# Optimization experiments

Hardware: AMD Instinct MI355X
Metric: run time of the kernel (lower is better)

The kernel has to match this reference:

```python
import jax, jax.numpy as jnp
import numpy as np

NUM_HEADS = 20
MAX_SEQLEN = 1500  # max per-segment length (Whisper 30s -> 1500 frames); static for jit
NEG = -1e30


def setup_inputs() -> dict:
    key = jax.random.key(0)
    ks = jax.random.split(key, 6)
    B, S, D = 4, MAX_SEQLEN, 1280
    T = B * S
    hidden_states = jax.random.normal(ks[0], (T, D), dtype=jnp.float32)
    # packed varlen layout: 4 equal-length audio segments
    cu_seqlens = (jnp.arange(B + 1, dtype=jnp.int32) * S)
    w = 0.02
    Wq = jax.random.normal(ks[1], (D, D), dtype=jnp.float32) * w
    Wk = jax.random.normal(ks[2], (D, D), dtype=jnp.float32) * w
    Wv = jax.random.normal(ks[3], (D, D), dtype=jnp.float32) * w
    Wo = jax.random.normal(ks[4], (D, D), dtype=jnp.float32) * w
    bq = jnp.zeros((D,), jnp.float32)
    bv = jnp.zeros((D,), jnp.float32)
    bo = jnp.zeros((D,), jnp.float32)
    return {"hidden_states": hidden_states, "cu_seqlens": cu_seqlens,
            "Wq": Wq, "bq": bq, "Wk": Wk, "Wv": Wv, "bv": bv, "Wo": Wo, "bo": bo}


def _varlen_attention(hidden_states, cu_seqlens, Wq, bq, Wk, Wv, bv, Wo, bo):
    T, D = hidden_states.shape
    H = NUM_HEADS
    d = D // H
    scale = d ** -0.5
    S = MAX_SEQLEN
    B = cu_seqlens.shape[0] - 1

    # projections (torch nn.Linear convention: y = x @ W.T + b; k_proj has no bias)
    q = hidden_states @ Wq.T + bq   # [T, D]
    k = hidden_states @ Wk.T        # [T, D]
    v = hidden_states @ Wv.T + bv   # [T, D]

    lens = cu_seqlens[1:] - cu_seqlens[:-1]                 # [B]
    pos = jnp.arange(S, dtype=jnp.int32)                    # [S]
    valid = pos[None, :] < lens[:, None]                    # [B, S]
    idx = cu_seqlens[:-1, None] + pos[None, :]              # [B, S]
    idx_g = jnp.where(valid, idx, 0)

    # unpack to padded [B, S, H, d]
    qb = q[idx_g].reshape(B, S, H, d)
    kb = k[idx_g].reshape(B, S, H, d)
    vb = v[idx_g].reshape(B, S, H, d)

    scores = jnp.einsum('bqhd,bkhd->bhqk', qb, kb) * scale  # [B, H, S, S]
    scores = jnp.where(valid[:, None, None, :], scores, NEG)
    attn = jax.nn.softmax(scores, axis=-1)
    out = jnp.einsum('bhqk,bkhd->bqhd', attn, vb).reshape(B, S, D)

    # repack to [T, D]; invalid slots scatter out-of-bounds and are dropped
    idx_s = jnp.where(valid, idx, T).reshape(-1)
    packed = jnp.zeros((T, D), out.dtype).at[idx_s].set(out.reshape(-1, D), mode='drop')
    return packed @ Wo.T + bo


def reference(hidden_states, cu_seqlens, Wq, bq, Wk, Wv, bv, Wo, bo):
    return _varlen_attention(hidden_states, cu_seqlens, Wq, bq, Wk, Wv, bv, Wo, bo)
```

## Files before the change

### kernel.cpp

```cpp
#include <hip/hip_runtime.h>
#include <stdint.h>
#include <math.h>

#define DMODEL 1280
#define NHEAD  20
#define DHEAD  64
#define NSEG   4
#define MAXS   1500
#define SPAD   1536
#define TPAD   (NSEG*SPAD)
#define QT128  ((MAXS + 127) / 128)
#define BM 128
#define BN 128
#define BK 32
#define QSCALE 0.18033688011112042f
#define NEGV  -1e30f

typedef float  f32x4  __attribute__((ext_vector_type(4)));
typedef __bf16 bf16x8 __attribute__((ext_vector_type(8)));

#if __has_builtin(__builtin_amdgcn_exp2f)
#define EXP2F(x) __builtin_amdgcn_exp2f(x)
#else
#define EXP2F(x) exp2f(x)
#endif

__device__ __forceinline__ ushort f2bf(float f) {
  union { float f; uint32_t u; } a; a.f = f;
  uint32_t u = a.u;
  u += 0x7FFFu + ((u >> 16) & 1u);
  return (ushort)(u >> 16);
}

__device__ __forceinline__ uint32_t pk2(float a, float b) {
  union { float f; uint32_t u; } ua, ub; ua.f = a; ub.f = b;
  uint32_t x = ua.u + 0x8000u, y = ub.u + 0x8000u;
  return (x >> 16) | (y & 0xFFFF0000u);
}

__device__ __forceinline__ void async16(const void* g, void* lds) {
  __builtin_amdgcn_global_load_lds((const __attribute__((address_space(1))) void*)g,
                                   (__attribute__((address_space(3))) void*)lds,
                                   16, 0, 0);
}

__device__ __forceinline__ int perm32(int a) {
  return ((a >> 2) & 3) * 8 + ((a >> 4) & 1) * 4 + (a & 3);
}

__global__ void __launch_bounds__(256)
cvt_all(const float* __restrict__ hs, const float* __restrict__ Wq,
        const float* __restrict__ Wk, const float* __restrict__ Wv,
        const float* __restrict__ Wo, ushort* __restrict__ dst, int nX, int DD) {
  const int i = (blockIdx.x * 256 + threadIdx.x) * 4;
  const float* src;
  if (i < nX) {
    src = hs + i;
  } else {
    int j = i - nX;
    const int z = (j >= DD) + (j >= 2 * DD) + (j >= 3 * DD);
    const float* w = (z == 0) ? Wq : (z == 1) ? Wk : (z == 2) ? Wv : Wo;
    src = w + (j - z * DD);
  }
  float4 v = *(const float4*)src;
  ushort4 o;
  o.x = f2bf(v.x); o.y = f2bf(v.y); o.z = f2bf(v.z); o.w = f2bf(v.w);
  *(ushort4*)(dst + i) = o;
}

__device__ __forceinline__ void gemm_tile_mainloop(
    const ushort* __restrict__ A, const ushort* __restrict__ W,
    int M, int m0, int n0, ushort* As, ushort* Bs, f32x4 (&acc)[4][4])
{
  const int tid  = threadIdx.x;
  const int wave = tid >> 6, lane = tid & 63;
  const int quad = lane >> 4, c16 = lane & 15;
  const int wr = (wave >> 1) * 64, wc = (wave & 1) * 64;

  const int M0 = wave * 128 + lane, M1 = M0 + 64;
  const int sr0 = M0 >> 3, pp0 = M0 & 7, p0 = pp0 ^ (sr0 & 7);
  const int sr1 = M1 >> 3, pp1 = M1 & 7, p1 = pp1 ^ (sr1 & 7);
  const int row0 = sr0 * 2 + (p0 >> 2), kc0 = (p0 & 3) << 3;
  const int row1 = sr1 * 2 + (p1 >> 2), kc1 = (p1 & 3) << 3;
  const ushort* Ap0 = A + (size_t)(m0 + row0) * DMODEL + kc0;
  const ushort* Ap1 = A + (size_t)(m0 + row1) * DMODEL + kc1;
  const ushort* Bp0 = W + (size_t)(n0 + row0) * DMODEL + kc0;
  const ushort* Bp1 = W + (size_t)(n0 + row1) * DMODEL + kc1;
  const int o0 = wave * 1024;
  const int o1 = wave * 1024 + 512;
  const int BUF = BM * BK;

  async16(Ap0, As + o0); async16(Ap1, As + o1);
  async16(Bp0, Bs + o0); async16(Bp1, Bs + o1);

  int c = 0;
  for (int k0 = 0; k0 < DMODEL; k0 += BK, c ^= 1) {
    __syncthreads();
    if (k0 + BK < DMODEL) {
      const int kn = k0 + BK;
      const int bo = (c ^ 1) * BUF;
      async16(Ap0 + kn, As + bo + o0); async16(Ap1 + kn, As + bo + o1);
      async16(Bp0 + kn, Bs + bo + o0); async16(Bp1 + kn, Bs + bo + o1);
    }
    const ushort* Ab = As + c * BUF;
    const ushort* Bb = Bs + c * BUF;
    bf16x8 a[4], b[4];
#pragma unroll
    for (int i = 0; i < 4; ++i) {
      const int row = wr + i * 16 + c16;
      const int sr = row >> 1;
      const int off = (sr << 6) + (((((row & 1) << 2) | quad) ^ (sr & 7)) << 3);
      a[i] = *(const bf16x8*)(Ab + off);
    }
#pragma unroll
    for (int j = 0; j < 4; ++j) {
      const int row = wc + j * 16 + c16;
      const int sr = row >> 1;
      const int off = (sr << 6) + (((((row & 1) << 2) | quad) ^ (sr & 7)) << 3);
      b[j] = *(const bf16x8*)(Bb + off);
    }
#pragma unroll
    for (int i = 0; i < 4; ++i)
#pragma unroll
      for (int j = 0; j < 4; ++j)
        acc[i][j] = __builtin_amdgcn_mfma_f32_16x16x32_bf16(a[i], b[j], acc[i][j], 0, 0, 0);
  }
}

__global__ void __launch_bounds__(256, 4)
gemm_qkv(const ushort* __restrict__ X, const ushort* __restrict__ W4,
         const float* __restrict__ bq, const float* __restrict__ bv,
         const int* __restrict__ cu,
         ushort* __restrict__ qb, ushort* __restrict__ kb, ushort* __restrict__ vt, int M)
{
  __shared__ ushort As[2 * BM * BK], Bs[2 * BN * BK];
  const int wg = blockIdx.x;
  if (wg >= 30) return;
  const int z = wg / 10;
  const int n0 = (wg % 10) * BN;
  const int m0 = blockIdx.y * BM;
  const ushort* W = W4 + (size_t)z * DMODEL * DMODEL;

  f32x4 acc[4][4];
  f32x4 zero = {0.f, 0.f, 0.f, 0.f};
#pragma unroll
  for (int i = 0; i < 4; ++i)
#pragma unroll
    for (int j = 0; j < 4; ++j) acc[i][j] = zero;

  gemm_tile_mainloop(X, W, M, m0, n0, As, Bs, acc);

  const int tid = threadIdx.x, wave = tid >> 6, lane = tid & 63;
  const int quad = lane >> 4, c16 = lane & 15;
  const int wr = (wave >> 1) * 64, wc = (wave & 1) * 64;

  if (z == 2) {
    const int c1 = cu[1], c2 = cu[2], c3 = cu[3];
#pragma unroll
    for (int i = 0; i < 4; ++i) {
      const int t0 = m0 + wr + i * 16 + quad * 4;
      const int s0a = (t0 >= c1) + (t0 >= c2) + (t0 >= c3);
      const int s3a = (t0 + 3 >= c1) + (t0 + 3 >= c2) + (t0 + 3 >= c3);
      const int seg0 = (s0a == 0) ? 0 : (s0a == 1) ? c1 : (s0a == 2) ? c2 : c3;
#pragma unroll
      for (int j = 0; j < 4; ++j) {
        const int cfeat = n0 + wc + j * 16 + c16;
        const float bb = bv[cfeat];
        if (t0 + 3 < M && s0a == s3a) {
          const int s = t0 - seg0;
          const size_t base = (size_t)cfeat * TPAD + (size_t)s0a * SPAD
                            + (size_t)(s & ~31) + perm32(s & 31);
          ushort4 w;
          w.x = f2bf(acc[i][j][0] + bb);
          w.y = f2bf(acc[i][j][1] + bb);
          w.z = f2bf(acc[i][j][2] + bb);
          w.w = f2bf(acc[i][j][3] + bb);
          *(ushort4*)(vt + base) = w;
        } else {
#pragma unroll
          for (int r = 0; r < 4; ++r) {
            const int t = t0 + r;
            if (t < M) {
              const int sb = (t >= c1) + (t >= c2) + (t >= c3);
              const int sg = (sb == 0) ? 0 : (sb == 1) ? c1 : (sb == 2) ? c2 : c3;
              const int s = t - sg;
              vt[(size_t)cfeat * TPAD + (size_t)sb * SPAD + (s & ~31) + perm32(s & 31)]
                  = f2bf(acc[i][j][r] + bb);
            }
          }
        }
      }
    }
  } else {
    ushort* out = (z == 0) ? qb : kb;
    const float* bias = (z == 0) ? bq : (const float*)nullptr;
    const float oscale = (z == 0) ? QSCALE : 1.0f;
#pragma unroll
    for (int i = 0; i < 4; ++i) {
      const int rbase = m0 + wr + i * 16 + quad * 4;
#pragma unroll
      for (int j = 0; j < 4; ++j) {
        const int c = n0 + wc + j * 16 + c16;
        const float bb = bias ? bias[c] : 0.f;
#pragma unroll
        for (int r = 0; r < 4; ++r) {
          const int rr = rbase + r;
          if (rr < M) out[(size_t)rr * DMODEL + c] = f2bf((acc[i][j][r] + bb) * oscale);
        }
      }
    }
  }
}

__global__ void __launch_bounds__(256, 4)
gemm_out(const ushort* __restrict__ A, const ushort* __restrict__ W,
         const float* __restrict__ bias, float* __restrict__ out, int M)
{
  __shared__ ushort As[2 * BM * BK], Bs[2 * BN * BK];
  const int wg = blockIdx.x;
  if (wg >= 10) return;
  const int n0 = wg * BN;
  const int m0 = blockIdx.y * BM;
  f32x4 acc[4][4];
  f32x4 zero = {0.f, 0.f, 0.f, 0.f};
#pragma unroll
  for (int i = 0; i < 4; ++i)
#pragma unroll
    for (int j = 0; j < 4; ++j) acc[i][j] = zero;

  gemm_tile_mainloop(A, W, M, m0, n0, As, Bs, acc);

  const int tid = threadIdx.x, wave = tid >> 6, lane = tid & 63;
  const int quad = lane >> 4, c16 = lane & 15;
  const int wr = (wave >> 1) * 64, wc = (wave & 1) * 64;
#pragma unroll
  for (int i = 0; i < 4; ++i) {
    const int rbase = m0 + wr + i * 16 + quad * 4;
#pragma unroll
    for (int j = 0; j < 4; ++j) {
      const int c = n0 + wc + j * 16 + c16;
      const float bb = bias[c];
#pragma unroll
      for (int r = 0; r < 4; ++r) {
        const int rr = rbase + r;
        if (rr < M) out[(size_t)rr * DMODEL + c] = acc[i][j][r] + bb;
      }
    }
  }
}

__global__ void __launch_bounds__(256, 4)
attn_fused(const ushort* __restrict__ qb, const ushort* __restrict__ kb,
           const ushort* __restrict__ vt, ushort* __restrict__ ob,
           const int* __restrict__ cu, int T)
{
  __shared__ ushort SB[2][8192];
  const int hs = blockIdx.x;
  const int b = hs / NHEAD, h = hs % NHEAD;
  const int seg0 = cu[b];
  const int len  = cu[b + 1] - seg0;
  const int q0 = blockIdx.y * 128;
  if (q0 >= len) return;
  const int tid = threadIdx.x, wave = tid >> 6, lane = tid & 63;
  const int quad = lane >> 4, c16 = lane & 15;

  {
    const int s = wave * 64 + lane;
#pragma unroll
    for (int t = 0; t < 4; ++t) {
      const int slot = t * 256 + s;
      const int r = slot >> 3, k2 = slot & 7;
      const int col = ((k2 ^ (r & 7)) << 3);
      async16(qb + (size_t)(seg0 + q0 + r) * DMODEL + h * DHEAD + col,
              &SB[0][(t * 256 + wave * 64) * 8]);
    }
  }

  const int sl  = wave * 64 + lane;
  const int rr0 = sl >> 3, kk2 = sl & 7;
  const int colc = ((kk2 ^ (rr0 & 7)) << 3);
  const ushort* kp0 = kb + (size_t)(seg0 + rr0) * DMODEL + h * DHEAD + colc;
  const ushort* kp1 = kp0 + (size_t)32 * DMODEL;
  const ushort* vp0 = vt + (size_t)(h * DHEAD + rr0) * TPAD + (size_t)b * SPAD + colc;
  const ushort* vp1 = vp0 + (size_t)32 * TPAD;
  const int ldo0 = wave * 512;
  const int ldo1 = 2048 + wave * 512;

  __syncthreads();

  bf16x8 aq[2][2];
#pragma unroll
  for (int n = 0; n < 2; ++n)
#pragma unroll
    for (int ks = 0; ks < 2; ++ks) {
      const int row = wave * 32 + n * 16 + c16;
      aq[n][ks] = *(const bf16x8*)(&SB[0][row * 64 + (((ks * 4 + quad) ^ (c16 & 7)) << 3)]);
    }

  async16(kp0, &SB[1][ldo0]);        async16(kp1, &SB[1][ldo1]);
  async16(vp0, &SB[1][4096 + ldo0]); async16(vp1, &SB[1][4096 + ldo1]);
  kp0 += (size_t)64 * DMODEL; kp1 += (size_t)64 * DMODEL; vp0 += 64; vp1 += 64;

  float l_i[2] = {0.f, 0.f};
  f32x4 o_acc[2][4];
  f32x4 zero = {0.f, 0.f, 0.f, 0.f};
#pragma unroll
  for (int n = 0; n < 2; ++n)
#pragma unroll
    for (int m = 0; m < 4; ++m) o_acc[n][m] = zero;

  const int niter = (len + 63) >> 6;
  for (int it = 0; it < niter; ++it) {
    __syncthreads();
    const ushort* Kt = &SB[1 ^ (it & 1)][0];
    const ushort* Vt = &SB[1 ^ (it & 1)][4096];

    if (it + 1 < niter) {
      ushort* Dst = &SB[it & 1][0];
      async16(kp0, Dst + ldo0);        async16(kp1, Dst + ldo1);
      async16(vp0, Dst + 4096 + ldo0); async16(vp1, Dst + 4096 + ldo1);
      kp0 += (size_t)64 * DMODEL; kp1 += (size_t)64 * DMODEL; vp0 += 64; vp1 += 64;
    }

    f32x4 s[2][4];
#pragma unroll
    for (int f = 0; f < 4; ++f) {
      const int row = f * 16 + c16;
      const int ch = c16 & 7;
      bf16x8 ak0 = *(const bf16x8*)(Kt + row * 64 + ((quad ^ ch) << 3));
      bf16x8 ak1 = *(const bf16x8*)(Kt + row * 64 + (((4 + quad) ^ ch) << 3));
#pragma unroll
      for (int n = 0; n < 2; ++n) {
        s[n][f] = zero;
        s[n][f] = __builtin_amdgcn_mfma_f32_16x16x32_bf16(ak0, aq[n][0], s[n][f], 0, 0, 0);
        s[n][f] = __builtin_amdgcn_mfma_f32_16x16x32_bf16(ak1, aq[n][1], s[n][f], 0, 0, 0);
      }
    }

    const int kv0 = it * 64;
    if (kv0 + 64 > len) {
#pragma unroll
      for (int f = 0; f < 4; ++f) {
        const int kvb = kv0 + f * 16 + quad * 4;
#pragma unroll
        for (int r = 0; r < 4; ++r)
          if (kvb + r >= len) { s[0][f][r] = NEGV; s[1][f][r] = NEGV; }
      }
    }

#pragma unroll
    for (int n = 0; n < 2; ++n) {
      float rs = 0.f;
#pragma unroll
      for (int f = 0; f < 4; ++f)
#pragma unroll
        for (int r = 0; r < 4; ++r) {
          const float p = EXP2F(s[n][f][r]);
          s[n][f][r] = p;
          rs += p;
        }
      l_i[n] += rs;
    }

    bf16x8 bp[2][2];
#pragma unroll
    for (int n = 0; n < 2; ++n)
#pragma unroll
      for (int g = 0; g < 2; ++g) {
        union { uint32_t u[4]; bf16x8 v; } cv;
        cv.u[0] = pk2(s[n][2 * g][0], s[n][2 * g][1]);
        cv.u[1] = pk2(s[n][2 * g][2], s[n][2 * g][3]);
        cv.u[2] = pk2(s[n][2 * g + 1][0], s[n][2 * g + 1][1]);
        cv.u[3] = pk2(s[n][2 * g + 1][2], s[n][2 * g + 1][3]);
        bp[n][g] = cv.v;
      }

#pragma unroll
    for (int m = 0; m < 4; ++m) {
      const int row = m * 16 + c16;
      const int ch = c16 & 7;
      bf16x8 av0 = *(const bf16x8*)(Vt + row * 64 + ((quad ^ ch) << 3));
      bf16x8 av1 = *(const bf16x8*)(Vt + row * 64 + (((4 + quad) ^ ch) << 3));
#pragma unroll
      for (int n = 0; n < 2; ++n) {
        o_acc[n][m] = __builtin_amdgcn_mfma_f32_16x16x32_bf16(av0, bp[n][0], o_acc[n][m], 0, 0, 0);
        o_acc[n][m] = __builtin_amdgcn_mfma_f32_16x16x32_bf16(av1, bp[n][1], o_acc[n][m], 0, 0, 0);
      }
    }
  }

#pragma unroll
  for (int n = 0; n < 2; ++n) {
    float l = l_i[n];
    l += __shfl_xor(l, 16);
    l += __shfl_xor(l, 32);
    const int q = q0 + wave * 32 + n * 16 + c16;
    if (q < len) {
      const float inv = 1.0f / l;
      const size_t base = (size_t)(seg0 + q) * DMODEL + h * DHEAD;
#pragma unroll
      for (int m = 0; m < 4; ++m) {
        ushort4 pk;
        pk.x = f2bf(o_acc[n][m][0] * inv);
        pk.y = f2bf(o_acc[n][m][1] * inv);
        pk.z = f2bf(o_acc[n][m][2] * inv);
        pk.w = f2bf(o_acc[n][m][3] * inv);
        *(ushort4*)(ob + base + m * 16 + quad * 4) = pk;
      }
    }
  }
}

extern "C" void kernel_launch(void* const* d_in, const int* in_sizes, int n_in,
                              void* d_out, int out_size, void* d_ws, size_t ws_size,
                              hipStream_t stream)
{
  (void)n_in; (void)out_size; (void)ws_size;
  const float* hs = (const float*)d_in[0];
  const int*   cu = (const int*)d_in[1];
  const float* Wq = (const float*)d_in[2];
  const float* bq = (const float*)d_in[3];
  const float* Wk = (const float*)d_in[4];
  const float* Wv = (const float*)d_in[5];
  const float* bv = (const float*)d_in[6];
  const float* Wo = (const float*)d_in[7];
  const float* bo = (const float*)d_in[8];
  float* out = (float*)d_out;
  const int T  = in_sizes[0] / DMODEL;
  const int DD = DMODEL * DMODEL;
  const int nX = T * DMODEL;

  ushort* ws  = (ushort*)d_ws;
  ushort* X   = ws;
  ushort* W4  = X + (size_t)nX;
  ushort* qb  = W4 + 4 * (size_t)DD;
  ushort* kb  = qb + (size_t)T * DMODEL;
  ushort* vt  = kb + (size_t)T * DMODEL;
  ushort* ob  = X;

  const int ncvt = nX + 4 * DD;
  cvt_all<<<(ncvt / 4 + 255) / 256, 256, 0, stream>>>(hs, Wq, Wk, Wv, Wo, ws, nX, DD);

  gemm_qkv<<<dim3(32, (T + BM - 1) / BM), 256, 0, stream>>>(
      X, W4, bq, bv, cu, qb, kb, vt, T);

  attn_fused<<<dim3(NSEG * NHEAD, QT128), 256, 0, stream>>>(qb, kb, vt, ob, cu, T);

  gemm_out<<<dim3(16, (T + BM - 1) / BM), 256, 0, stream>>>(
      ob, W4 + 3 * (size_t)DD, bo, out, T);
}
```

Baseline: 307.2 us.

## Fuse Q/K/V projections into one block sharing the activation tile

Each QKV GEMM block now computes the Q, K and V outputs for the same 128x128 tile, loading the activation tile once and reusing it across all three weight tiles. Each block holds three accumulator sets and a larger LDS weight buffer, and occupancy is lowered to 2 blocks per SM. This removes the triplicated activation loads and shrinks the grid from 30 to 10 active column blocks. In exchange there are fewer blocks to fill the GPU, 470 in total, and the higher register and LDS use per block may hurt latency hiding.

```diff
diff --git a/kernel.cpp b/kernel.cpp
--- a/kernel.cpp
+++ b/kernel.cpp
@@ -68,10 +68,162 @@
   *(ushort4*)(dst + i) = o;
 }
 
-__device__ __forceinline__ void gemm_tile_mainloop(
-    const ushort* __restrict__ A, const ushort* __restrict__ W,
-    int M, int m0, int n0, ushort* As, ushort* Bs, f32x4 (&acc)[4][4])
+__global__ void __launch_bounds__(256, 2)
+gemm_qkv(const ushort* __restrict__ X, const ushort* __restrict__ W4,
+         const float* __restrict__ bq, const float* __restrict__ bv,
+         const int* __restrict__ cu,
+         ushort* __restrict__ qb, ushort* __restrict__ kb, ushort* __restrict__ vt, int M)
 {
+  __shared__ ushort As[2 * 4096];
+  __shared__ ushort Bs[2 * 3 * 4096];
+  const int wg = blockIdx.x;
+  if (wg >= 10) return;
+  const int n0 = wg * BN;
+  const int m0 = blockIdx.y * BM;
+  const int DD = DMODEL * DMODEL;
+
+  const int tid  = threadIdx.x;
+  const int wave = tid >> 6, lane = tid & 63;
+  const int quad = lane >> 4, c16 = lane & 15;
+  const int wr = (wave >> 1) * 64, wc = (wave & 1) * 64;
+
+  const int M0 = wave * 128 + lane, M1 = M0 + 64;
+  const int sr0 = M0 >> 3, pp0 = M0 & 7, p0 = pp0 ^ (sr0 & 7);
+  const int sr1 = M1 >> 3, pp1 = M1 & 7, p1 = pp1 ^ (sr1 & 7);
+  const int row0 = sr0 * 2 + (p0 >> 2), kc0 = (p0 & 3) << 3;
+  const int row1 = sr1 * 2 + (p1 >> 2), kc1 = (p1 & 3) << 3;
+  const ushort* Ap0 = X + (size_t)(m0 + row0) * DMODEL + kc0;
+  const ushort* Ap1 = X + (size_t)(m0 + row1) * DMODEL + kc1;
+  const ushort* Bq0 = W4 + (size_t)(n0 + row0) * DMODEL + kc0;
+  const ushort* Bq1 = W4 + (size_t)(n0 + row1) * DMODEL + kc1;
+  const int o0 = wave * 1024;
+  const int o1 = wave * 1024 + 512;
+
+  async16(Ap0, As + o0); async16(Ap1, As + o1);
+#pragma unroll
+  for (int z = 0; z < 3; ++z) {
+    async16(Bq0 + (size_t)z * DD, Bs + z * 4096 + o0);
+    async16(Bq1 + (size_t)z * DD, Bs + z * 4096 + o1);
+  }
+
+  f32x4 acc[3][4][4];
+  f32x4 zero = {0.f, 0.f, 0.f, 0.f};
+#pragma unroll
+  for (int z = 0; z < 3; ++z)
+#pragma unroll
+    for (int i = 0; i < 4; ++i)
+#pragma unroll
+      for (int j = 0; j < 4; ++j) acc[z][i][j] = zero;
+
+  int c = 0;
+  for (int k0 = 0; k0 < DMODEL; k0 += BK, c ^= 1) {
+    __syncthreads();
+    if (k0 + BK < DMODEL) {
+      const int kn = k0 + BK;
+      const int ba = (c ^ 1) * 4096;
+      const int bb = (c ^ 1) * 12288;
+      async16(Ap0 + kn, As + ba + o0); async16(Ap1 + kn, As + ba + o1);
+#pragma unroll
+      for (int z = 0; z < 3; ++z) {
+        async16(Bq0 + (size_t)z * DD + kn, Bs + bb + z * 4096 + o0);
+        async16(Bq1 + (size_t)z * DD + kn, Bs + bb + z * 4096 + o1);
+      }
+    }
+    const ushort* Ab = As + c * 4096;
+    bf16x8 a[4];
+#pragma unroll
+    for (int i = 0; i < 4; ++i) {
+      const int row = wr + i * 16 + c16;
+      const int sr = row >> 1;
+      const int off = (sr << 6) + (((((row & 1) << 2) | quad) ^ (sr & 7)) << 3);
+      a[i] = *(const bf16x8*)(Ab + off);
+    }
+#pragma unroll
+    for (int z = 0; z < 3; ++z) {
+      const ushort* Bb = Bs + c * 12288 + z * 4096;
+      bf16x8 b[4];
+#pragma unroll
+      for (int j = 0; j < 4; ++j) {
+        const int row = wc + j * 16 + c16;
+        const int sr = row >> 1;
+        const int off = (sr << 6) + (((((row & 1) << 2) | quad) ^ (sr & 7)) << 3);
+        b[j] = *(const bf16x8*)(Bb + off);
+      }
+#pragma unroll
+      for (int i = 0; i < 4; ++i)
+#pragma unroll
+        for (int j = 0; j < 4; ++j)
+          acc[z][i][j] = __builtin_amdgcn_mfma_f32_16x16x32_bf16(a[i], b[j], acc[z][i][j], 0, 0, 0);
+    }
+  }
+
+#pragma unroll
+  for (int i = 0; i < 4; ++i) {
+    const int rbase = m0 + wr + i * 16 + quad * 4;
+#pragma unroll
+    for (int j = 0; j < 4; ++j) {
+      const int col = n0 + wc + j * 16 + c16;
+      const float bbq = bq[col];
+#pragma unroll
+      for (int r = 0; r < 4; ++r) {
+        const int rr = rbase + r;
+        if (rr < M) {
+          qb[(size_t)rr * DMODEL + col] = f2bf((acc[0][i][j][r] + bbq) * QSCALE);
+          kb[(size_t)rr * DMODEL + col] = f2bf(acc[1][i][j][r]);
+        }
+      }
+    }
+  }
+  {
+    const int c1 = cu[1], c2 = cu[2], c3 = cu[3];
+#pragma unroll
+    for (int i = 0; i < 4; ++i) {
+      const int t0 = m0 + wr + i * 16 + quad * 4;
+      const int s0a = (t0 >= c1) + (t0 >= c2) + (t0 >= c3);
+      const int s3a = (t0 + 3 >= c1) + (t0 + 3 >= c2) + (t0 + 3 >= c3);
+      const int seg0 = (s0a == 0) ? 0 : (s0a == 1) ? c1 : (s0a == 2) ? c2 : c3;
+#pragma unroll
+      for (int j = 0; j < 4; ++j) {
+        const int cfeat = n0 + wc + j * 16 + c16;
+        const float bb = bv[cfeat];
+        if (t0 + 3 < M && s0a == s3a) {
+          const int s = t0 - seg0;
+          const size_t base = (size_t)cfeat * TPAD + (size_t)s0a * SPAD
+                            + (size_t)(s & ~31) + perm32(s & 31);
+          ushort4 w;
+          w.x = f2bf(acc[2][i][j][0] + bb);
+          w.y = f2bf(acc[2][i][j][1] + bb);
+          w.z = f2bf(acc[2][i][j][2] + bb);
+          w.w = f2bf(acc[2][i][j][3] + bb);
+          *(ushort4*)(vt + base) = w;
+        } else {
+#pragma unroll
+          for (int r = 0; r < 4; ++r) {
+            const int t = t0 + r;
+            if (t < M) {
+              const int sb = (t >= c1) + (t >= c2) + (t >= c3);
+              const int sg = (sb == 0) ? 0 : (sb == 1) ? c1 : (sb == 2) ? c2 : c3;
+              const int s = t - sg;
+              vt[(size_t)cfeat * TPAD + (size_t)sb * SPAD + (s & ~31) + perm32(s & 31)]
+                  = f2bf(acc[2][i][j][r] + bb);
+            }
+          }
+        }
+      }
+    }
+  }
+}
+
+__global__ void __launch_bounds__(256, 4)
+gemm_out(const ushort* __restrict__ A, const ushort* __restrict__ W,
+         const float* __restrict__ bias, float* __restrict__ out, int M)
+{
+  __shared__ ushort As[2 * BM * BK], Bs[2 * BN * BK];
+  const int wg = blockIdx.x;
+  if (wg >= 10) return;
+  const int n0 = wg * BN;
+  const int m0 = blockIdx.y * BM;
+
   const int tid  = threadIdx.x;
   const int wave = tid >> 6, lane = tid & 63;
   const int quad = lane >> 4, c16 = lane & 15;
@@ -93,6 +245,13 @@
   async16(Ap0, As + o0); async16(Ap1, As + o1);
   async16(Bp0, Bs + o0); async16(Bp1, Bs + o1);
 
+  f32x4 acc[4][4];
+  f32x4 zero = {0.f, 0.f, 0.f, 0.f};
+#pragma unroll
+  for (int i = 0; i < 4; ++i)
+#pragma unroll
+    for (int j = 0; j < 4; ++j) acc[i][j] = zero;
+
   int c = 0;
   for (int k0 = 0; k0 < DMODEL; k0 += BK, c ^= 1) {
     __syncthreads();
@@ -125,125 +284,19 @@
       for (int j = 0; j < 4; ++j)
         acc[i][j] = __builtin_amdgcn_mfma_f32_16x16x32_bf16(a[i], b[j], acc[i][j], 0, 0, 0);
   }
-}
-
-__global__ void __launch_bounds__(256, 4)
-gemm_qkv(const ushort* __restrict__ X, const ushort* __restrict__ W4,
-         const float* __restrict__ bq, const float* __restrict__ bv,
-         const int* __restrict__ cu,
-         ushort* __restrict__ qb, ushort* __restrict__ kb, ushort* __restrict__ vt, int M)
-{
-  __shared__ ushort As[2 * BM * BK], Bs[2 * BN * BK];
-  const int wg = blockIdx.x;
-  if (wg >= 30) return;
-  const int z = wg / 10;
-  const int n0 = (wg % 10) * BN;
-  const int m0 = blockIdx.y * BM;
-  const ushort* W = W4 + (size_t)z * DMODEL * DMODEL;
-
-  f32x4 acc[4][4];
-  f32x4 zero = {0.f, 0.f, 0.f, 0.f};
-#pragma unroll
-  for (int i = 0; i < 4; ++i)
-#pragma unroll
-    for (int j = 0; j < 4; ++j) acc[i][j] = zero;
-
-  gemm_tile_mainloop(X, W, M, m0, n0, As, Bs, acc);
-
-  const int tid = threadIdx.x, wave = tid >> 6, lane = tid & 63;
-  const int quad = lane >> 4, c16 = lane & 15;
-  const int wr = (wave >> 1) * 64, wc = (wave & 1) * 64;
-
-  if (z == 2) {
-    const int c1 = cu[1], c2 = cu[2], c3 = cu[3];
-#pragma unroll
-    for (int i = 0; i < 4; ++i) {
-      const int t0 = m0 + wr + i * 16 + quad * 4;
-      const int s0a = (t0 >= c1) + (t0 >= c2) + (t0 >= c3);
-      const int s3a = (t0 + 3 >= c1) + (t0 + 3 >= c2) + (t0 + 3 >= c3);
-      const int seg0 = (s0a == 0) ? 0 : (s0a == 1) ? c1 : (s0a == 2) ? c2 : c3;
-#pragma unroll
-      for (int j = 0; j < 4; ++j) {
-        const int cfeat = n0 + wc + j * 16 + c16;
-        const float bb = bv[cfeat];
-        if (t0 + 3 < M && s0a == s3a) {
-          const int s = t0 - seg0;
-          const size_t base = (size_t)cfeat * TPAD + (size_t)s0a * SPAD
-                            + (size_t)(s & ~31) + perm32(s & 31);
-          ushort4 w;
-          w.x = f2bf(acc[i][j][0] + bb);
-          w.y = f2bf(acc[i][j][1] + bb);
-          w.z = f2bf(acc[i][j][2] + bb);
-          w.w = f2bf(acc[i][j][3] + bb);
-          *(ushort4*)(vt + base) = w;
-        } else {
-#pragma unroll
-          for (int r = 0; r < 4; ++r) {
-            const int t = t0 + r;
-            if (t < M) {
-              const int sb = (t >= c1) + (t >= c2) + (t >= c3);
-              const int sg = (sb == 0) ? 0 : (sb == 1) ? c1 : (sb == 2) ? c2 : c3;
-              const int s = t - sg;
-              vt[(size_t)cfeat * TPAD + (size_t)sb * SPAD + (s & ~31) + perm32(s & 31)]
-                  = f2bf(acc[i][j][r] + bb);
-            }
-          }
-        }
-      }
-    }
-  } else {
-    ushort* out = (z == 0) ? qb : kb;
-    const float* bias = (z == 0) ? bq : (const float*)nullptr;
-    const float oscale = (z == 0) ? QSCALE : 1.0f;
-#pragma unroll
-    for (int i = 0; i < 4; ++i) {
-      const int rbase = m0 + wr + i * 16 + quad * 4;
-#pragma unroll
-      for (int j = 0; j < 4; ++j) {
-        const int c = n0 + wc + j * 16 + c16;
-        const float bb = bias ? bias[c] : 0.f;
-#pragma unroll
-        for (int r = 0; r < 4; ++r) {
-          const int rr = rbase + r;
-          if (rr < M) out[(size_t)rr * DMODEL + c] = f2bf((acc[i][j][r] + bb) * oscale);
-        }
-      }
-    }
-  }
-}
-
-__global__ void __launch_bounds__(256, 4)
-gemm_out(const ushort* __restrict__ A, const ushort* __restrict__ W,
-         const float* __restrict__ bias, float* __restrict__ out, int M)
-{
-  __shared__ ushort As[2 * BM * BK], Bs[2 * BN * BK];
-  const int wg = blockIdx.x;
-  if (wg >= 10) return;
-  const int n0 = wg * BN;
-  const int m0 = blockIdx.y * BM;
-  f32x4 acc[4][4];
-  f32x4 zero = {0.f, 0.f, 0.f, 0.f};
-#pragma unroll
-  for (int i = 0; i < 4; ++i)
-#pragma unroll
-    for (int j = 0; j < 4; ++j) acc[i][j] = zero;
-
-  gemm_tile_mainloop(A, W, M, m0, n0, As, Bs, acc);
-
-  const int tid = threadIdx.x, wave = tid >> 6, lane = tid & 63;
-  const int quad = lane >> 4, c16 = lane & 15;
-  const int wr = (wave >> 1) * 64, wc = (wave & 1) * 64;
+
+  const int tidw = wr, wcn = wc;
 #pragma unroll
   for (int i = 0; i < 4; ++i) {
-    const int rbase = m0 + wr + i * 16 + quad * 4;
+    const int rbase = m0 + tidw + i * 16 + quad * 4;
 #pragma unroll
     for (int j = 0; j < 4; ++j) {
-      const int c = n0 + wc + j * 16 + c16;
-      const float bb = bias[c];
+      const int col = n0 + wcn + j * 16 + c16;
+      const float bb = bias[col];
 #pragma unroll
       for (int r = 0; r < 4; ++r) {
         const int rr = rbase + r;
-        if (rr < M) out[(size_t)rr * DMODEL + c] = acc[i][j][r] + bb;
+        if (rr < M) out[(size_t)rr * DMODEL + col] = acc[i][j][r] + bb;
       }
     }
   }
@@ -441,7 +494,7 @@
   const int ncvt = nX + 4 * DD;
   cvt_all<<<(ncvt / 4 + 255) / 256, 256, 0, stream>>>(hs, Wq, Wk, Wv, Wo, ws, nX, DD);
 
-  gemm_qkv<<<dim3(32, (T + BM - 1) / BM), 256, 0, stream>>>(
+  gemm_qkv<<<dim3(16, (T + BM - 1) / BM), 256, 0, stream>>>(
       X, W4, bq, bv, cu, qb, kb, vt, T);
 
   attn_fused<<<dim3(NSEG * NHEAD, QT128), 256, 0, stream>>>(qb, kb, vt, ob, cu, T);
```

Measured after the change: 342.6 us. +11.5%, slower.
